# Kernel optimization log

Measured on AMD Instinct MI355X. Metric: run time of the kernel, lower is better.

## Reference

```python
import jax, jax.numpy as jnp
import numpy as np

D_MODEL = 256
N_HEAD = 8
D_FF = 2048
B, N = 8, 1024
NEG = -9e15
EPS = 1e-5


def _layernorm(x, g, b):
    mu = jnp.mean(x, axis=-1, keepdims=True)
    var = jnp.mean(jnp.square(x - mu), axis=-1, keepdims=True)
    return (x - mu) * jax.lax.rsqrt(var + EPS) * g + b


def setup_inputs() -> dict:
    key = jax.random.key(0)
    ks = jax.random.split(key, 12)
    d, dff = D_MODEL, D_FF
    s = 1.0 / np.sqrt(d)
    inp = {
        "src": jax.random.normal(ks[0], (B, N, d), dtype=jnp.float32),
        "adj": jax.random.randint(ks[1], (B, N, N), 0, 2, dtype=jnp.int32),
        "W_gat": jax.random.normal(ks[2], (d, d), dtype=jnp.float32) * s,
        "a_gat": jax.random.normal(ks[3], (2 * d, 1), dtype=jnp.float32) * s,
        "in_proj_w": jax.random.normal(ks[4], (3 * d, d), dtype=jnp.float32) * s,
        "in_proj_b": jnp.zeros((3 * d,), dtype=jnp.float32),
        "out_proj_w": jax.random.normal(ks[5], (d, d), dtype=jnp.float32) * s,
        "out_proj_b": jnp.zeros((d,), dtype=jnp.float32),
        "lin1_w": jax.random.normal(ks[6], (dff, d), dtype=jnp.float32) * s,
        "lin1_b": jnp.zeros((dff,), dtype=jnp.float32),
        "lin2_w": jax.random.normal(ks[7], (d, dff), dtype=jnp.float32) * (1.0 / np.sqrt(dff)),
        "lin2_b": jnp.zeros((d,), dtype=jnp.float32),
        "ln1_g": jnp.ones((d,), dtype=jnp.float32),
        "ln1_b": jnp.zeros((d,), dtype=jnp.float32),
        "ln2_g": jnp.ones((d,), dtype=jnp.float32),
        "ln2_b": jnp.zeros((d,), dtype=jnp.float32),
        "ln3_g": jnp.ones((d,), dtype=jnp.float32),
        "ln3_b": jnp.zeros((d,), dtype=jnp.float32),
    }
    return inp


def reference(src, adj, W_gat, a_gat, in_proj_w, in_proj_b, out_proj_w, out_proj_b,
              lin1_w, lin1_b, lin2_w, lin2_b, ln1_g, ln1_b, ln2_g, ln2_b, ln3_g, ln3_b):
    d = D_MODEL
    # --- Graph attention (dropout inactive in eval) ---
    Wh = jnp.matmul(src, W_gat)                      # [B,N,d]
    a1 = a_gat[:d, 0]
    a2 = a_gat[d:, 0]
    # e[b,i,j] = Wh_i . a1 + Wh_j . a2  (equivalent to concat+matmul in source)
    f1 = Wh @ a1                                     # [B,N]
    f2 = Wh @ a2                                     # [B,N]
    e = f1[:, :, None] + f2[:, None, :]              # [B,N,N]
    e = jnp.where(adj > 0, e, NEG)
    attn = jax.nn.softmax(e, axis=-1)
    h_prime = jnp.matmul(attn, Wh)                   # [B,N,d]
    graph_out = jax.nn.elu(h_prime)
    x = _layernorm(src + graph_out, ln1_g, ln1_b)

    # --- Multi-head self-attention ---
    qkv = x @ in_proj_w.T + in_proj_b                # [B,N,3d]
    q, k, v = jnp.split(qkv, 3, axis=-1)
    hd = d // N_HEAD
    def heads(t):
        return t.reshape(B, N, N_HEAD, hd).transpose(0, 2, 1, 3)  # [B,H,N,hd]
    q, k, v = heads(q), heads(k), heads(v)
    scores = jnp.einsum("bhid,bhjd->bhij", q, k) / np.sqrt(hd)
    probs = jax.nn.softmax(scores, axis=-1)
    ctx = jnp.einsum("bhij,bhjd->bhid", probs, v)
    ctx = ctx.transpose(0, 2, 1, 3).reshape(B, N, d)
    attn_out = ctx @ out_proj_w.T + out_proj_b
    y = _layernorm(x + attn_out, ln2_g, ln2_b)

    # --- FFN ---
    ff = jax.nn.relu(y @ lin1_w.T + lin1_b) @ lin2_w.T + lin2_b
    return _layernorm(y + ff, ln3_g, ln3_b)
```

## Files before the change

### kernel.cpp

```cpp
#include <hip/hip_runtime.h>
#include <math.h>

constexpr int BATCH = 8;
constexpr int SEQ   = 1024;
constexpr int DM    = 256;
constexpr int DF    = 2048;
constexpr int NH    = 8;
constexpr int HDIM  = 32;
constexpr int ROWS  = BATCH * SEQ;
constexpr float NEGV = -9e15f;
constexpr float EPSV = 1e-5f;
constexpr float QSCALE = 0.2550351822f;
constexpr float LOG2E  = 1.44269504f;

typedef __attribute__((ext_vector_type(8))) short short8;
typedef __attribute__((ext_vector_type(4))) float f32x4;

static __device__ __forceinline__ ushort f2bf(float f) {
    unsigned x = __float_as_uint(f);
    unsigned r = (x + 0x7fffu + ((x >> 16) & 1u)) >> 16;
    return (ushort)r;
}
static __device__ __forceinline__ float bf2f(ushort u) {
    return __uint_as_float((unsigned)u << 16);
}
static __device__ __forceinline__ unsigned cvt_pk_bf16(float lo, float hi) {
    unsigned r;
    asm volatile("v_cvt_pk_bf16_f32 %0, %1, %2" : "=v"(r) : "v"(lo), "v"(hi));
    return r;
}

struct CastArgs {
    const float* in[5];
    ushort* out[5];
    int n4[5];
};
constexpr int CAST_BLKS = (2097152 + 196608 + 65536 + 524288 + 524288) / 4 / 256;

__global__ __launch_bounds__(256) void prep_k(CastArgs a,
                                              const float* __restrict__ W_gat,
                                              const float* __restrict__ a_gat,
                                              ushort* __restrict__ wgTb,
                                              float* __restrict__ w1,
                                              float* __restrict__ w2)
{
    __shared__ float Ts[32][33];
    const int bid = blockIdx.x;
    const int t = threadIdx.x;

    if (bid < CAST_BLKS) {
        int idx = bid * 256 + t;
        #pragma unroll
        for (int r = 0; r < 5; r++) {
            if (idx < a.n4[r]) {
                float4 v = *(const float4*)&a.in[r][(size_t)idx * 4];
                ushort4 o; o.x = f2bf(v.x); o.y = f2bf(v.y); o.z = f2bf(v.z); o.w = f2bf(v.w);
                *(ushort4*)&a.out[r][(size_t)idx * 4] = o;
                return;
            }
            idx -= a.n4[r];
        }
    } else if (bid < CAST_BLKS + 64) {
        const int bb = bid - CAST_BLKS;
        const int r0 = (bb >> 3) * 32, c0 = (bb & 7) * 32;
        const int lr = t >> 3, lc4 = (t & 7) * 4;
        float4 v = *(const float4*)&W_gat[(size_t)(r0 + lr) * DM + c0 + lc4];
        Ts[lr][lc4] = v.x; Ts[lr][lc4 + 1] = v.y; Ts[lr][lc4 + 2] = v.z; Ts[lr][lc4 + 3] = v.w;
        __syncthreads();
        const int oc = t >> 3, or4 = (t & 7) * 4;
        ushort4 o;
        o.x = f2bf(Ts[or4 + 0][oc]); o.y = f2bf(Ts[or4 + 1][oc]);
        o.z = f2bf(Ts[or4 + 2][oc]); o.w = f2bf(Ts[or4 + 3][oc]);
        *(ushort4*)&wgTb[(size_t)(c0 + oc) * DM + r0 + or4] = o;
    } else {
        const int k = (bid - CAST_BLKS - 64) * 4 + (t >> 6);
        const int l = t & 63;
        float4 wv = *(const float4*)&W_gat[(size_t)k * DM + 4 * l];
        float4 a1 = *(const float4*)&a_gat[4 * l];
        float4 a2 = *(const float4*)&a_gat[DM + 4 * l];
        float s1 = wv.x*a1.x + wv.y*a1.y + wv.z*a1.z + wv.w*a1.w;
        float s2 = wv.x*a2.x + wv.y*a2.y + wv.z*a2.z + wv.w*a2.w;
        #pragma unroll
        for (int off = 32; off; off >>= 1) {
            s1 += __shfl_xor(s1, off, 64);
            s2 += __shfl_xor(s2, off, 64);
        }
        if (l == 0) { w1[k] = s1; w2[k] = s2; }
    }
}

__global__ __launch_bounds__(256) void f12_k(const float* __restrict__ src,
                                             const float* __restrict__ w1,
                                             const float* __restrict__ w2,
                                             float* __restrict__ f1,
                                             float* __restrict__ f2)
{
    const size_t row = (size_t)blockIdx.x * 4 + (threadIdx.x >> 6);
    const int l = threadIdx.x & 63;
    float4 sv = *(const float4*)&src[row * DM + 4 * l];
    float4 v1 = *(const float4*)&w1[4 * l];
    float4 v2 = *(const float4*)&w2[4 * l];
    float s1 = sv.x*v1.x + sv.y*v1.y + sv.z*v1.z + sv.w*v1.w;
    float s2 = sv.x*v2.x + sv.y*v2.y + sv.z*v2.z + sv.w*v2.w;
    #pragma unroll
    for (int off = 32; off; off >>= 1) {
        s1 += __shfl_xor(s1, off, 64);
        s2 += __shfl_xor(s2, off, 64);
    }
    if (l == 0) { f1[row] = s1 * LOG2E; f2[row] = s2 * LOG2E; }
}

template<int EP, int BM, int BN>
__global__ __launch_bounds__(256) void gemm_bf(const ushort* __restrict__ A,
                                               const ushort* __restrict__ B,
                                               const float* __restrict__ bias,
                                               ushort* __restrict__ Cb,
                                               int N, int K, int ldB,
                                               long long sA, long long sB, long long sC)
{
    __shared__ ushort As[2][BM][40];
    __shared__ ushort Bs[2][BN][40];
    A += (size_t)blockIdx.z * sA;
    B += (size_t)blockIdx.z * sB;

    const int t  = threadIdx.x;
    const int m0 = blockIdx.y * BM, n0 = blockIdx.x * BN;
    const int lane = t & 63, lo = lane & 15, hi = lane >> 4;
    const int w = t >> 6;
    constexpr int NI = BM / 32, NJ = BN / 32;
    const int wr = (w >> 1) * (BM / 2);
    const int wc = (w & 1) * (BN / 2);

    const int lrA = (BM == 128) ? (t >> 1) : (t >> 2);
    const int lcA = (BM == 128) ? ((t & 1) * 16) : ((t & 3) * 8);
    const int lrB = (BN == 128) ? (t >> 1) : (t >> 2);
    const int lcB = (BN == 128) ? ((t & 1) * 16) : ((t & 3) * 8);

    f32x4 acc[NI][NJ];
    const f32x4 zero = {0.f, 0.f, 0.f, 0.f};
    #pragma unroll
    for (int i = 0; i < NI; i++)
        #pragma unroll
        for (int j = 0; j < NJ; j++) acc[i][j] = zero;

    const ushort* Ap = A + (size_t)(m0 + lrA) * K + lcA;
    const ushort* Bp = B + (size_t)(n0 + lrB) * ldB + lcB;

    short8 ar0, ar1, br0, br1;
    ar0 = *(const short8*)(Ap);
    if constexpr (BM == 128) ar1 = *(const short8*)(Ap + 8);
    br0 = *(const short8*)(Bp);
    if constexpr (BN == 128) br1 = *(const short8*)(Bp + 8);
    *(short8*)&As[0][lrA][lcA] = ar0;
    if constexpr (BM == 128) *(short8*)&As[0][lrA][lcA + 8] = ar1;
    *(short8*)&Bs[0][lrB][lcB] = br0;
    if constexpr (BN == 128) *(short8*)&Bs[0][lrB][lcB + 8] = br1;

    const int NT = K >> 5;
    for (int it = 0; it < NT; it++) {
        const int cur = it & 1;
        if (it + 1 < NT) {
            const int k0 = (it + 1) << 5;
            ar0 = *(const short8*)(Ap + k0);
            if constexpr (BM == 128) ar1 = *(const short8*)(Ap + k0 + 8);
            br0 = *(const short8*)(Bp + k0);
            if constexpr (BN == 128) br1 = *(const short8*)(Bp + k0 + 8);
        }
        __syncthreads();

        short8 afr[NI], bfr[NJ];
        #pragma unroll
        for (int i = 0; i < NI; i++) afr[i] = *(const short8*)&As[cur][wr + i*16 + lo][hi * 8];
        #pragma unroll
        for (int j = 0; j < NJ; j++) bfr[j] = *(const short8*)&Bs[cur][wc + j*16 + lo][hi * 8];
        #pragma unroll
        for (int i = 0; i < NI; i++)
            #pragma unroll
            for (int j = 0; j < NJ; j++)
                acc[i][j] = __builtin_amdgcn_mfma_f32_16x16x32_bf16(afr[i], bfr[j], acc[i][j], 0, 0, 0);

        if (it + 1 < NT) {
            *(short8*)&As[cur ^ 1][lrA][lcA] = ar0;
            if constexpr (BM == 128) *(short8*)&As[cur ^ 1][lrA][lcA + 8] = ar1;
            *(short8*)&Bs[cur ^ 1][lrB][lcB] = br0;
            if constexpr (BN == 128) *(short8*)&Bs[cur ^ 1][lrB][lcB + 8] = br1;
        }
    }

    Cb += (size_t)blockIdx.z * sC;
    #pragma unroll
    for (int j = 0; j < NJ; j++) {
        const int col = n0 + wc + j * 16 + lo;
        float bj = (EP == 1 || EP == 2 || EP == 6) ? bias[col] : 0.f;
        #pragma unroll
        for (int i = 0; i < NI; i++) {
            const int rbase = m0 + wr + i * 16 + hi * 4;
            #pragma unroll
            for (int r = 0; r < 4; r++) {
                float v = acc[i][j][r] + bj;
                if (EP == 3) v = v > 0.f ? v : expm1f(v);
                if (EP == 2) v = fmaxf(v, 0.f);
                if (EP == 6 && col < DM) v *= QSCALE;
                Cb[(size_t)(rbase + r) * N + col] = f2bf(v);
            }
        }
    }
}

template<int MODE>
__global__ __launch_bounds__(256) void ln_k(const float* __restrict__ af,
                                            const ushort* __restrict__ ab,
                                            const ushort* __restrict__ r,
                                            const float* __restrict__ g,
                                            const float* __restrict__ be,
                                            float* __restrict__ of,
                                            ushort* __restrict__ ob)
{
    const size_t row = (size_t)blockIdx.x * 4 + (threadIdx.x >> 6);
    const int l = threadIdx.x & 63;
    ushort4 rv = *(const ushort4*)&r[row * DM + 4 * l];
    float v0, v1, v2, v3;
    if (MODE == 0) {
        float4 av = *(const float4*)&af[row * DM + 4 * l];
        v0 = av.x + bf2f(rv.x); v1 = av.y + bf2f(rv.y);
        v2 = av.z + bf2f(rv.z); v3 = av.w + bf2f(rv.w);
    } else {
        ushort4 av = *(const ushort4*)&ab[row * DM + 4 * l];
        v0 = bf2f(av.x) + bf2f(rv.x); v1 = bf2f(av.y) + bf2f(rv.y);
        v2 = bf2f(av.z) + bf2f(rv.z); v3 = bf2f(av.w) + bf2f(rv.w);
    }
    float s = (v0 + v1) + (v2 + v3);
    #pragma unroll
    for (int off = 32; off; off >>= 1) s += __shfl_xor(s, off, 64);
    const float mu = s * (1.0f / DM);
    float q = (v0-mu)*(v0-mu) + (v1-mu)*(v1-mu) + (v2-mu)*(v2-mu) + (v3-mu)*(v3-mu);
    #pragma unroll
    for (int off = 32; off; off >>= 1) q += __shfl_xor(q, off, 64);
    const float rs = rsqrtf(q * (1.0f / DM) + EPSV);
    float4 gv = *(const float4*)&g[4 * l];
    float4 bv = *(const float4*)&be[4 * l];
    float o0 = (v0 - mu) * rs * gv.x + bv.x;
    float o1 = (v1 - mu) * rs * gv.y + bv.y;
    float o2 = (v2 - mu) * rs * gv.z + bv.z;
    float o3 = (v3 - mu) * rs * gv.w + bv.w;
    if (MODE == 2) {
        float4 ov; ov.x = o0; ov.y = o1; ov.z = o2; ov.w = o3;
        *(float4*)&of[row * DM + 4 * l] = ov;
    } else {
        ushort4 obv;
        obv.x = f2bf(o0); obv.y = f2bf(o1); obv.z = f2bf(o2); obv.w = f2bf(o3);
        *(ushort4*)&ob[row * DM + 4 * l] = obv;
    }
}

__global__ __launch_bounds__(256) void gat_sm_k(const int* __restrict__ adj,
                                                const float* __restrict__ f1,
                                                const float* __restrict__ f2,
                                                ushort* __restrict__ P)
{
    const int row = blockIdx.x * 4 + (threadIdx.x >> 6);
    const int b = row >> 10;
    const int l = threadIdx.x & 63;
    const int* arow = adj + (size_t)row * SEQ;
    const float* f2b = f2 + ((size_t)b << 10);
    const float f1i = f1[row];

    float e[16];
    float mx = -3.4e38f;
    #pragma unroll
    for (int u = 0; u < 4; u++) {
        const int j = 4 * l + 256 * u;
        int4 a4 = *(const int4*)&arow[j];
        float4 f4 = *(const float4*)&f2b[j];
        e[4*u+0] = a4.x > 0 ? f1i + f4.x : NEGV;
        e[4*u+1] = a4.y > 0 ? f1i + f4.y : NEGV;
        e[4*u+2] = a4.z > 0 ? f1i + f4.z : NEGV;
        e[4*u+3] = a4.w > 0 ? f1i + f4.w : NEGV;
        mx = fmaxf(mx, fmaxf(fmaxf(e[4*u], e[4*u+1]), fmaxf(e[4*u+2], e[4*u+3])));
    }
    #pragma unroll
    for (int off = 32; off; off >>= 1) mx = fmaxf(mx, __shfl_xor(mx, off, 64));
    float s = 0.f;
    #pragma unroll
    for (int k = 0; k < 16; k++) { e[k] = exp2f(e[k] - mx); s += e[k]; }
    #pragma unroll
    for (int off = 32; off; off >>= 1) s += __shfl_xor(s, off, 64);
    const float inv = 1.0f / s;
    #pragma unroll
    for (int u = 0; u < 4; u++) {
        ushort4 o;
        o.x = f2bf(e[4*u+0] * inv); o.y = f2bf(e[4*u+1] * inv);
        o.z = f2bf(e[4*u+2] * inv); o.w = f2bf(e[4*u+3] * inv);
        *(ushort4*)&P[(size_t)row * SEQ + 4 * l + 256 * u] = o;
    }
}

__device__ __forceinline__ int vt_idx(int d, int kv) { return d * 72 + ((d >> 3) & 3) * 16 + kv; }
constexpr int VTSZ = 32 * 72 + 3 * 16 + 8;

__global__ __launch_bounds__(512) void mha_k(const ushort* __restrict__ qkv,
                                             ushort* __restrict__ ctxb)
{
    __shared__ ushort Ks[2][64][40];
    __shared__ ushort Vt[2][VTSZ];
    __shared__ ushort Ps[128][72];

    const int blk = blockIdx.x;
    const int grp = blk & 63, qt = blk >> 6;
    const int h = grp & 7, b = grp >> 3;
    const int i0 = qt << 7;
    const int t = threadIdx.x;
    const int w = t >> 6, lane = t & 63, lo = lane & 15, hi = lane >> 4;
    const int gsh = lane & 48;
    const size_t base = (size_t)b * SEQ * 768;

    const short8 aQ = *(const short8*)(qkv + base + (size_t)(i0 + 16*w + lo) * 768 + h * HDIM + hi * 8);
    short8 ones;
    #pragma unroll
    for (int e = 0; e < 8; e++) ones[e] = (short)0x3F80;

    const int tt = t & 255;
    const int srow = tt >> 2, scb = (tt & 3) << 3;
    const bool isK = t < 256;
    const int vcol = (srow & 32) | ((srow & 15) << 1) | ((srow >> 4) & 1);
    {
        const ushort* p0 = qkv + base + (size_t)srow * 768 + h * HDIM + (isK ? 256 : 512) + scb;
        short8 v0 = *(const short8*)p0;
        if (isK) *(short8*)&Ks[0][srow][scb] = v0;
        else {
            #pragma unroll
            for (int e = 0; e < 8; e++) Vt[0][vt_idx(scb + e, vcol)] = (ushort)v0[e];
        }
    }

    float m_run[4], l_run[4];
    f32x4 O0 = {0.f, 0.f, 0.f, 0.f}, O1 = {0.f, 0.f, 0.f, 0.f};
    #pragma unroll
    for (int r = 0; r < 4; r++) { m_run[r] = -3.0e38f; l_run[r] = 0.f; }
    const f32x4 zero = {0.f, 0.f, 0.f, 0.f};

    short8 reg;
    for (int it = 0; it < 16; it++) {
        const int cur = it & 1;
        if (it < 15)
            reg = *(const short8*)(qkv + base + (size_t)((it + 1) * 64 + srow) * 768
                                   + h * HDIM + (isK ? 256 : 512) + scb);
        __syncthreads();

        f32x4 S[4];
        #pragma unroll
        for (int jt = 0; jt < 4; jt++) {
            short8 bK = *(const short8*)&Ks[cur][16 * jt + lo][hi * 8];
            S[jt] = __builtin_amdgcn_mfma_f32_16x16x32_bf16(aQ, bK, zero, 0, 0, 0);
        }

        float mxl[4];
        bool any = false;
        #pragma unroll
        for (int r = 0; r < 4; r++) {
            mxl[r] = fmaxf(fmaxf(S[0][r], S[1][r]), fmaxf(S[2][r], S[3][r]));
            any = any || (mxl[r] > m_run[r] + 8.f);
        }
        unsigned long long bal = __ballot(any);
        if ((bal >> gsh) & 0xffffULL) {
            #pragma unroll
            for (int r = 0; r < 4; r++) {
                float mx = mxl[r];
                #pragma unroll
                for (int off = 8; off; off >>= 1) mx = fmaxf(mx, __shfl_xor(mx, off, 16));
                float mnew = fmaxf(m_run[r], mx);
                float sc = exp2f(m_run[r] - mnew);
                m_run[r] = mnew;
                l_run[r] *= sc; O0[r] *= sc; O1[r] *= sc;
            }
        }
        #pragma unroll
        for (int r = 0; r < 4; r++) {
            const int row = 16 * w + 4 * hi + r;
            unsigned u01 = cvt_pk_bf16(exp2f(S[0][r] - m_run[r]), exp2f(S[1][r] - m_run[r]));
            unsigned u23 = cvt_pk_bf16(exp2f(S[2][r] - m_run[r]), exp2f(S[3][r] - m_run[r]));
            *(unsigned*)&Ps[row][2 * lo]      = u01;
            *(unsigned*)&Ps[row][32 + 2 * lo] = u23;
        }

        f32x4 O2 = zero;
        #pragma unroll
        for (int kt = 0; kt < 2; kt++) {
            short8 aP  = *(const short8*)&Ps[16 * w + lo][32 * kt + hi * 8];
            short8 bV0 = *(const short8*)&Vt[cur][vt_idx(lo,      32 * kt + hi * 8)];
            short8 bV1 = *(const short8*)&Vt[cur][vt_idx(16 + lo, 32 * kt + hi * 8)];
            O0 = __builtin_amdgcn_mfma_f32_16x16x32_bf16(aP, bV0, O0, 0, 0, 0);
            O1 = __builtin_amdgcn_mfma_f32_16x16x32_bf16(aP, bV1, O1, 0, 0, 0);
            O2 = __builtin_amdgcn_mfma_f32_16x16x32_bf16(aP, ones, O2, 0, 0, 0);
        }
        #pragma unroll
        for (int r = 0; r < 4; r++) l_run[r] += O2[r];

        if (it < 15) {
            if (isK) *(short8*)&Ks[cur ^ 1][srow][scb] = reg;
            else {
                #pragma unroll
                for (int e = 0; e < 8; e++) Vt[cur ^ 1][vt_idx(scb + e, vcol)] = (ushort)reg[e];
            }
        }
    }

    #pragma unroll
    for (int r = 0; r < 4; r++) {
        float inv = 1.0f / l_run[r];
        size_t row = (size_t)b * SEQ + i0 + 16 * w + 4 * hi + r;
        ctxb[row * DM + h * HDIM + lo]      = f2bf(O0[r] * inv);
        ctxb[row * DM + h * HDIM + 16 + lo] = f2bf(O1[r] * inv);
    }
}

extern "C" void kernel_launch(void* const* d_in, const int* in_sizes, int n_in,
                              void* d_out, int out_size, void* d_ws, size_t ws_size,
                              hipStream_t stream)
{
    const float* src        = (const float*)d_in[0];
    const int*   adj        = (const int*)  d_in[1];
    const float* W_gat      = (const float*)d_in[2];
    const float* a_gat      = (const float*)d_in[3];
    const float* in_proj_w  = (const float*)d_in[4];
    const float* in_proj_b  = (const float*)d_in[5];
    const float* out_proj_w = (const float*)d_in[6];
    const float* out_proj_b = (const float*)d_in[7];
    const float* lin1_w     = (const float*)d_in[8];
    const float* lin1_b     = (const float*)d_in[9];
    const float* lin2_w     = (const float*)d_in[10];
    const float* lin2_b     = (const float*)d_in[11];
    const float* ln1_g      = (const float*)d_in[12];
    const float* ln1_b_     = (const float*)d_in[13];
    const float* ln2_g      = (const float*)d_in[14];
    const float* ln2_b_     = (const float*)d_in[15];
    const float* ln3_g      = (const float*)d_in[16];
    const float* ln3_b_     = (const float*)d_in[17];

    char* base = (char*)d_ws;
    const size_t MB = 1024 * 1024;
    ushort* tmpb  = (ushort*)(base + 0 * MB);
    ushort* P_bf  = (ushort*)(base + 4 * MB);
    ushort* qkvb  = (ushort*)(base + 4 * MB);
    ushort* ff1b  = (ushort*)(base + 4 * MB);
    ushort* srcb  = (ushort*)(base + 36 * MB);
    ushort* WhTb  = (ushort*)(base + 40 * MB);
    ushort* xb    = (ushort*)(base + 44 * MB);
    ushort* yb    = (ushort*)(base + 48 * MB);
    ushort* ctxb  = (ushort*)(base + 52 * MB);
    float*  f1    = (float*) (base + 56 * MB);
    float*  f2    = f1 + ROWS;
    float*  w1    = f2 + ROWS;
    float*  w2    = w1 + DM;
    ushort* wgTb  = (ushort*)(base + 57 * MB);
    ushort* ipwb  = wgTb + 65536;
    ushort* opwb  = ipwb + 196608;
    ushort* l1wb  = opwb + 65536;
    ushort* l2wb  = l1wb + 524288;

    dim3 b256(256);

    CastArgs ca;
    ca.in[0] = src;       ca.out[0] = srcb; ca.n4[0] = 2097152 / 4;
    ca.in[1] = in_proj_w; ca.out[1] = ipwb; ca.n4[1] = 196608 / 4;
    ca.in[2] = out_proj_w;ca.out[2] = opwb; ca.n4[2] = 65536 / 4;
    ca.in[3] = lin1_w;    ca.out[3] = l1wb; ca.n4[3] = 524288 / 4;
    ca.in[4] = lin2_w;    ca.out[4] = l2wb; ca.n4[4] = 524288 / 4;
    prep_k<<<CAST_BLKS + 64 + 64, b256, 0, stream>>>(ca, W_gat, a_gat, wgTb, w1, w2);

    f12_k<<<ROWS / 4, b256, 0, stream>>>(src, w1, w2, f1, f2);
    gemm_bf<5, 64, 64><<<dim3(ROWS/64, DM/64, 1), b256, 0, stream>>>(wgTb, srcb, nullptr, WhTb,
                                                                     ROWS, DM, DM, 0, 0, 0);
    gat_sm_k<<<ROWS / 4, b256, 0, stream>>>(adj, f1, f2, P_bf);
    gemm_bf<3, 64, 64><<<dim3(DM/64, SEQ/64, 8), b256, 0, stream>>>(P_bf, WhTb, nullptr, tmpb,
                                                                    DM, SEQ, ROWS,
                                                                    (long long)SEQ * SEQ, (long long)SEQ, (long long)SEQ * DM);
    ln_k<0><<<ROWS / 4, b256, 0, stream>>>(src, nullptr, tmpb, ln1_g, ln1_b_, nullptr, xb);

    gemm_bf<6, 128, 64><<<dim3(768/64, ROWS/128, 1), b256, 0, stream>>>(xb, ipwb, in_proj_b, qkvb,
                                                                        768, DM, DM, 0, 0, 0);
    mha_k<<<BATCH * NH * (SEQ / 128), dim3(512), 0, stream>>>(qkvb, ctxb);
    gemm_bf<1, 64, 64><<<dim3(DM/64, ROWS/64, 1), b256, 0, stream>>>(ctxb, opwb, out_proj_b, tmpb,
                                                                     DM, DM, DM, 0, 0, 0);
    ln_k<1><<<ROWS / 4, b256, 0, stream>>>(nullptr, xb, tmpb, ln2_g, ln2_b_, nullptr, yb);

    gemm_bf<2, 128, 128><<<dim3(DF/128, ROWS/128, 1), b256, 0, stream>>>(yb, l1wb, lin1_b, ff1b,
                                                                         DF, DM, DM, 0, 0, 0);
    gemm_bf<1, 64, 64><<<dim3(DM/64, ROWS/64, 1), b256, 0, stream>>>(ff1b, l2wb, lin2_b, tmpb,
                                                                     DM, DF, DF, 0, 0, 0);
    ln_k<2><<<ROWS / 4, b256, 0, stream>>>(nullptr, yb, tmpb, ln3_g, ln3_b_, (float*)d_out, nullptr);
}
```

Measured before the change: 155.8 us.

## Fuse GAT masked softmax and aggregation GEMM into flash-style kernel

Replaces the separate GAT softmax kernel, which wrote a dense bf16 probability matrix, and the batched P·Wh GEMM with a single online-softmax kernel. Each block handles 16 rows, streams adjacency and WhT tiles through shared memory, rescales the running max lazily, and uses an MFMA against a ones vector for the row sums. This removes the 16 MB probability write and read-back plus one launch. In exchange it uses a small 16-row tile with 512 blocks and a larger shared memory footprint, which may limit occupancy and reuse of Wh tiles.

```diff
diff --git a/kernel.cpp b/kernel.cpp
--- a/kernel.cpp
+++ b/kernel.cpp
@@ -115,13 +115,10 @@
                                                const ushort* __restrict__ B,
                                                const float* __restrict__ bias,
                                                ushort* __restrict__ Cb,
-                                               int N, int K, int ldB,
-                                               long long sA, long long sB, long long sC)
+                                               int N, int K, int ldB)
 {
     __shared__ ushort As[2][BM][40];
     __shared__ ushort Bs[2][BN][40];
-    A += (size_t)blockIdx.z * sA;
-    B += (size_t)blockIdx.z * sB;
 
     const int t  = threadIdx.x;
     const int m0 = blockIdx.y * BM, n0 = blockIdx.x * BN;
@@ -187,7 +184,6 @@
         }
     }
 
-    Cb += (size_t)blockIdx.z * sC;
     #pragma unroll
     for (int j = 0; j < NJ; j++) {
         const int col = n0 + wc + j * 16 + lo;
@@ -198,11 +194,146 @@
             #pragma unroll
             for (int r = 0; r < 4; r++) {
                 float v = acc[i][j][r] + bj;
-                if (EP == 3) v = v > 0.f ? v : expm1f(v);
                 if (EP == 2) v = fmaxf(v, 0.f);
                 if (EP == 6 && col < DM) v *= QSCALE;
                 Cb[(size_t)(rbase + r) * N + col] = f2bf(v);
             }
+        }
+    }
+}
+
+__global__ __launch_bounds__(256) void gat_k(const int* __restrict__ adj,
+                                             const float* __restrict__ f1,
+                                             const float* __restrict__ f2,
+                                             const ushort* __restrict__ WhT,
+                                             ushort* __restrict__ out)
+{
+    __shared__ ushort Ws[256][72];
+    __shared__ int    adjS[16][68];
+    __shared__ ushort Ps[16][72];
+    __shared__ float  f2S[1024];
+    __shared__ float  f1S[16];
+
+    const int blk = blockIdx.x;
+    const int brow0 = blk << 4;
+    const int b = brow0 >> 10;
+    const size_t bcol = (size_t)b << 10;
+    const int t = threadIdx.x;
+    const int w = t >> 6, lane = t & 63, lo = lane & 15, hi = lane >> 4;
+    const int gsh = lane & 48;
+
+    *(float4*)&f2S[4 * t] = *(const float4*)&f2[bcol + 4 * t];
+    if (t < 16) f1S[t] = f1[brow0 + t];
+
+    short8 ones;
+    #pragma unroll
+    for (int e = 0; e < 8; e++) ones[e] = (short)0x3F80;
+
+    const int sd = t >> 3, sc = (t & 7) * 8;
+    const int ar = t >> 4, ac = (t & 15) * 4;
+
+    short8 wreg[8]; int4 areg;
+    auto load = [&](int j0) {
+        #pragma unroll
+        for (int p = 0; p < 8; p++)
+            wreg[p] = *(const short8*)(WhT + (size_t)(p * 32 + sd) * ROWS + bcol + j0 + sc);
+        areg = *(const int4*)(adj + (size_t)(brow0 + ar) * SEQ + j0 + ac);
+    };
+    auto store = [&]() {
+        #pragma unroll
+        for (int p = 0; p < 8; p++)
+            *(short8*)&Ws[p * 32 + sd][sc] = wreg[p];
+        *(int4*)&adjS[ar][ac] = areg;
+    };
+
+    float m_run[4], l_run[4];
+    f32x4 O[4];
+    const f32x4 zero = {0.f, 0.f, 0.f, 0.f};
+    #pragma unroll
+    for (int r = 0; r < 4; r++) { m_run[r] = -3.0e38f; l_run[r] = 0.f; }
+    #pragma unroll
+    for (int fr = 0; fr < 4; fr++) O[fr] = zero;
+
+    load(0);
+    store();
+
+    for (int it = 0; it < 16; it++) {
+        __syncthreads();
+        if (it < 15) load((it + 1) << 6);
+
+        const int j0 = it << 6;
+        float f1v[4];
+        #pragma unroll
+        for (int r = 0; r < 4; r++) f1v[r] = f1S[4 * hi + r];
+        float S[4][4];
+        #pragma unroll
+        for (int jt = 0; jt < 4; jt++) {
+            const float f2v = f2S[j0 + lo + 16 * jt];
+            #pragma unroll
+            for (int r = 0; r < 4; r++) {
+                int a = adjS[4 * hi + r][lo + 16 * jt];
+                S[jt][r] = (a > 0) ? (f1v[r] + f2v) : NEGV;
+            }
+        }
+        float mxl[4]; bool any = false;
+        #pragma unroll
+        for (int r = 0; r < 4; r++) {
+            mxl[r] = fmaxf(fmaxf(S[0][r], S[1][r]), fmaxf(S[2][r], S[3][r]));
+            any = any || (mxl[r] > m_run[r] + 8.f);
+        }
+        unsigned long long bal = __ballot(any);
+        if ((bal >> gsh) & 0xffffULL) {
+            #pragma unroll
+            for (int r = 0; r < 4; r++) {
+                float mx = mxl[r];
+                #pragma unroll
+                for (int off = 8; off; off >>= 1) mx = fmaxf(mx, __shfl_xor(mx, off, 16));
+                float mnew = fmaxf(m_run[r], mx);
+                float sc_ = exp2f(m_run[r] - mnew);
+                m_run[r] = mnew;
+                l_run[r] *= sc_;
+                #pragma unroll
+                for (int fr = 0; fr < 4; fr++) O[fr][r] *= sc_;
+            }
+        }
+        #pragma unroll
+        for (int r = 0; r < 4; r++) {
+            const int row = 4 * hi + r;
+            unsigned u01 = cvt_pk_bf16(exp2f(S[0][r] - m_run[r]), exp2f(S[1][r] - m_run[r]));
+            unsigned u23 = cvt_pk_bf16(exp2f(S[2][r] - m_run[r]), exp2f(S[3][r] - m_run[r]));
+            Ps[row][lo]      = (ushort)u01;
+            Ps[row][lo + 16] = (ushort)(u01 >> 16);
+            Ps[row][lo + 32] = (ushort)u23;
+            Ps[row][lo + 48] = (ushort)(u23 >> 16);
+        }
+
+        f32x4 O2 = zero;
+        #pragma unroll
+        for (int kt = 0; kt < 2; kt++) {
+            short8 aP = *(const short8*)&Ps[lo][kt * 32 + hi * 8];
+            #pragma unroll
+            for (int fr = 0; fr < 4; fr++) {
+                short8 bV = *(const short8*)&Ws[w * 64 + fr * 16 + lo][kt * 32 + hi * 8];
+                O[fr] = __builtin_amdgcn_mfma_f32_16x16x32_bf16(aP, bV, O[fr], 0, 0, 0);
+            }
+            O2 = __builtin_amdgcn_mfma_f32_16x16x32_bf16(aP, ones, O2, 0, 0, 0);
+        }
+        #pragma unroll
+        for (int r = 0; r < 4; r++) l_run[r] += O2[r];
+
+        __syncthreads();
+        if (it < 15) store();
+    }
+
+    #pragma unroll
+    for (int r = 0; r < 4; r++) {
+        const float inv = 1.0f / l_run[r];
+        const size_t row = (size_t)brow0 + 4 * hi + r;
+        #pragma unroll
+        for (int fr = 0; fr < 4; fr++) {
+            float v = O[fr][r] * inv;
+            v = v > 0.f ? v : expm1f(v);
+            out[row * DM + w * 64 + fr * 16 + lo] = f2bf(v);
         }
     }
 }
@@ -250,48 +381,6 @@
         ushort4 obv;
         obv.x = f2bf(o0); obv.y = f2bf(o1); obv.z = f2bf(o2); obv.w = f2bf(o3);
         *(ushort4*)&ob[row * DM + 4 * l] = obv;
-    }
-}
-
-__global__ __launch_bounds__(256) void gat_sm_k(const int* __restrict__ adj,
-                                                const float* __restrict__ f1,
-                                                const float* __restrict__ f2,
-                                                ushort* __restrict__ P)
-{
-    const int row = blockIdx.x * 4 + (threadIdx.x >> 6);
-    const int b = row >> 10;
-    const int l = threadIdx.x & 63;
-    const int* arow = adj + (size_t)row * SEQ;
-    const float* f2b = f2 + ((size_t)b << 10);
-    const float f1i = f1[row];
-
-    float e[16];
-    float mx = -3.4e38f;
-    #pragma unroll
-    for (int u = 0; u < 4; u++) {
-        const int j = 4 * l + 256 * u;
-        int4 a4 = *(const int4*)&arow[j];
-        float4 f4 = *(const float4*)&f2b[j];
-        e[4*u+0] = a4.x > 0 ? f1i + f4.x : NEGV;
-        e[4*u+1] = a4.y > 0 ? f1i + f4.y : NEGV;
-        e[4*u+2] = a4.z > 0 ? f1i + f4.z : NEGV;
-        e[4*u+3] = a4.w > 0 ? f1i + f4.w : NEGV;
-        mx = fmaxf(mx, fmaxf(fmaxf(e[4*u], e[4*u+1]), fmaxf(e[4*u+2], e[4*u+3])));
-    }
-    #pragma unroll
-    for (int off = 32; off; off >>= 1) mx = fmaxf(mx, __shfl_xor(mx, off, 64));
-    float s = 0.f;
-    #pragma unroll
-    for (int k = 0; k < 16; k++) { e[k] = exp2f(e[k] - mx); s += e[k]; }
-    #pragma unroll
-    for (int off = 32; off; off >>= 1) s += __shfl_xor(s, off, 64);
-    const float inv = 1.0f / s;
-    #pragma unroll
-    for (int u = 0; u < 4; u++) {
-        ushort4 o;
-        o.x = f2bf(e[4*u+0] * inv); o.y = f2bf(e[4*u+1] * inv);
-        o.z = f2bf(e[4*u+2] * inv); o.w = f2bf(e[4*u+3] * inv);
-        *(ushort4*)&P[(size_t)row * SEQ + 4 * l + 256 * u] = o;
     }
 }
 
@@ -440,7 +529,6 @@
     char* base = (char*)d_ws;
     const size_t MB = 1024 * 1024;
     ushort* tmpb  = (ushort*)(base + 0 * MB);
-    ushort* P_bf  = (ushort*)(base + 4 * MB);
     ushort* qkvb  = (ushort*)(base + 4 * MB);
     ushort* ff1b  = (ushort*)(base + 4 * MB);
     ushort* srcb  = (ushort*)(base + 36 * MB);
@@ -470,23 +558,20 @@
 
     f12_k<<<ROWS / 4, b256, 0, stream>>>(src, w1, w2, f1, f2);
     gemm_bf<5, 64, 64><<<dim3(ROWS/64, DM/64, 1), b256, 0, stream>>>(wgTb, srcb, nullptr, WhTb,
-                                                                     ROWS, DM, DM, 0, 0, 0);
-    gat_sm_k<<<ROWS / 4, b256, 0, stream>>>(adj, f1, f2, P_bf);
-    gemm_bf<3, 64, 64><<<dim3(DM/64, SEQ/64, 8), b256, 0, stream>>>(P_bf, WhTb, nullptr, tmpb,
-                                                                    DM, SEQ, ROWS,
-                                                                    (long long)SEQ * SEQ, (long long)SEQ, (long long)SEQ * DM);
+                                                                     ROWS, DM, DM);
+    gat_k<<<ROWS / 16, b256, 0, stream>>>(adj, f1, f2, WhTb, tmpb);
     ln_k<0><<<ROWS / 4, b256, 0, stream>>>(src, nullptr, tmpb, ln1_g, ln1_b_, nullptr, xb);
 
     gemm_bf<6, 128, 64><<<dim3(768/64, ROWS/128, 1), b256, 0, stream>>>(xb, ipwb, in_proj_b, qkvb,
-                                                                        768, DM, DM, 0, 0, 0);
+                                                                        768, DM, DM);
     mha_k<<<BATCH * NH * (SEQ / 128), dim3(512), 0, stream>>>(qkvb, ctxb);
     gemm_bf<1, 64, 64><<<dim3(DM/64, ROWS/64, 1), b256, 0, stream>>>(ctxb, opwb, out_proj_b, tmpb,
-                                                                     DM, DM, DM, 0, 0, 0);
+                                                                     DM, DM, DM);
     ln_k<1><<<ROWS / 4, b256, 0, stream>>>(nullptr, xb, tmpb, ln2_g, ln2_b_, nullptr, yb);
 
     gemm_bf<2, 128, 128><<<dim3(DF/128, ROWS/128, 1), b256, 0, stream>>>(yb, l1wb, lin1_b, ff1b,
-                                                                         DF, DM, DM, 0, 0, 0);
+                                                                         DF, DM, DM);
     gemm_bf<1, 64, 64><<<dim3(DM/64, ROWS/64, 1), b256, 0, stream>>>(ff1b, l2wb, lin2_b, tmpb,
-                                                                     DM, DF, DF, 0, 0, 0);
+                                                                     DM, DF, DF);
     ln_k<2><<<ROWS / 4, b256, 0, stream>>>(nullptr, yb, tmpb, ln3_g, ln3_b_, (float*)d_out, nullptr);
 }
```

Measured after the change: 163.1 us. 1.05x slower.
